# Kernel optimization log

Hardware: AMD Instinct MI355X
Metric: run time of the kernel (lower is better)

The kernel has to match this reference:

```python
import jax, jax.numpy as jnp
from jax import lax
import numpy as np

NEG = -1e9  # -inf surrogate for DP boundaries (matches deepblast's large-negative init)


def _lstm(xe, W_ih, W_hh, b):
    # xe: (B, T, D) -> hidden states (B, T, H). Single-layer LSTM via lax.scan.
    B, T, _ = xe.shape
    H = W_hh.shape[0]
    pre = xe @ W_ih + b  # precompute input contributions: (B, T, 4H)
    def step(carry, p):
        h, c = carry
        z = p + h @ W_hh
        i, f, g, o = jnp.split(z, 4, axis=-1)
        c = jax.nn.sigmoid(f) * c + jax.nn.sigmoid(i) * jnp.tanh(g)
        h = jax.nn.sigmoid(o) * jnp.tanh(c)
        return (h, c), h
    h0 = jnp.zeros((B, H), xe.dtype)
    _, hs = lax.scan(step, (h0, h0), jnp.swapaxes(pre, 0, 1))
    return jnp.swapaxes(hs, 0, 1)


def _embed(tok, emb, W_ih, W_hh, b_lstm, W_out, b_out):
    # StackedRNN: token embedding -> LSTM -> linear projection to nembed
    return _lstm(emb[tok], W_ih, W_hh, b_lstm) @ W_out + b_out


def _nw(theta, A):
    # Softmax-relaxed Needleman-Wunsch terminal value, anti-diagonal wavefront scan.
    # V[i,j] = theta[i-1,j-1] + logsumexp(V[i-1,j-1], V[i-1,j]+A, V[i,j-1]+A)
    B, N, M = theta.shape
    ii = jnp.arange(N + 1)
    d0 = jnp.full((B, N + 1), NEG, theta.dtype).at[:, 0].set(0.0)  # diag k=0: V[0,0]=0
    d1 = jnp.full((B, N + 1), NEG, theta.dtype)                    # diag k=1: boundaries
    def shift(a):  # a[i] -> a[i-1]
        return jnp.concatenate([jnp.full((a.shape[0], 1), NEG, a.dtype), a[:, :-1]], axis=1)
    def step(carry, k):
        p2, p1 = carry  # diagonals k-2, k-1; entry i holds V[i, (k-2)-i] / V[i, (k-1)-i]
        jj = k - ii
        valid = (ii >= 1) & (ii <= N) & (jj >= 1) & (jj <= M)
        td = theta[:, jnp.clip(ii - 1, 0, N - 1), jnp.clip(jj - 1, 0, M - 1)]  # (B, N+1)
        v = jax.nn.logsumexp(jnp.stack([shift(p1) + A, shift(p2), p1 + A], 0), axis=0)
        cur = jnp.where(valid[None, :], td + v, NEG)
        return (p1, cur), None
    (_, last), _ = lax.scan(step, (d0, d1), jnp.arange(2, N + M + 1))
    return last[:, N]  # V[N, M] per batch


def setup_inputs() -> dict:
    key = jax.random.key(0)
    ks = jax.random.split(key, 10)
    B, T, V, E, H = 32, 512, 22, 512, 512
    return {
        "x": jax.random.randint(ks[0], (B, T), 0, V),
        "y": jax.random.randint(ks[1], (B, T), 0, V),
        "emb": jax.random.normal(ks[2], (V, E), jnp.float32) * 0.1,
        "W_ih": jax.random.normal(ks[3], (E, 4 * H), jnp.float32) * 0.05,
        "W_hh": jax.random.normal(ks[4], (H, 4 * H), jnp.float32) * 0.05,
        "b_lstm": jnp.zeros((4 * H,), jnp.float32),
        "W_out": jax.random.normal(ks[5], (H, E), jnp.float32) * 0.05,
        "b_out": jnp.zeros((E,), jnp.float32),
        "W_gap": jax.random.normal(ks[6], (2 * E, 1), jnp.float32) * 0.05,
        "b_gap": jnp.zeros((1,), jnp.float32),
    }


def reference(x, y, emb, W_ih, W_hh, b_lstm, W_out, b_out, W_gap, b_gap):
    zx = _embed(x, emb, W_ih, W_hh, b_lstm, W_out, b_out)  # (B, N, E)
    zy = _embed(y, emb, W_ih, W_hh, b_lstm, W_out, b_out)  # (B, M, E)
    theta = jnp.einsum('bid,bjd->bij', zx, zy)             # (B, N, M)
    merged = jnp.concatenate([zx.mean(1), zy.mean(1)], axis=1)
    A = merged @ W_gap + b_gap                             # (B, 1) learned gap score
    return _nw(theta, A)                                   # (B,) DP terminal value
```

## Files before the change

kernel.cpp:

```cpp
#include <hip/hip_runtime.h>
#include <math.h>

#define TSEQ 512
#define HDIM 512
#define EDIM 512
#define NB   32
#define ROWS 64
#define GATES 2048
#define NEGV -1000000000.0f

typedef __attribute__((ext_vector_type(8))) short bf16x8;
typedef __attribute__((ext_vector_type(4))) float f32x4;

__device__ __forceinline__ float sigf(float x){ return __builtin_amdgcn_rcpf(1.0f + __expf(-x)); }

__device__ __forceinline__ float tanhfast(float x){
  float t = __expf(-2.0f*fabsf(x));
  float r = (1.0f - t)*__builtin_amdgcn_rcpf(1.0f + t);
  return copysignf(r, x);
}

__device__ __forceinline__ unsigned short f2bf(float f){
  unsigned int u = __builtin_bit_cast(unsigned int, f);
  unsigned int r = (u + 0x7fff + ((u>>16)&1)) >> 16;
  return (unsigned short)r;
}

__device__ __forceinline__ float bf2f(unsigned short v){
  unsigned int u = ((unsigned int)v)<<16;
  return __builtin_bit_cast(float, u);
}

__global__ __launch_bounds__(256) void table_k(const float* __restrict__ emb,
        const float* __restrict__ W_ih, const float* __restrict__ b_lstm,
        float* __restrict__ table){
  int j = blockIdx.x*256 + threadIdx.x;
  int v = blockIdx.y;
  float acc = b_lstm[j];
  #pragma unroll 4
  for(int k=0;k<EDIM;k++) acc = fmaf(emb[v*EDIM+k], W_ih[(size_t)k*GATES+j], acc);
  table[(size_t)v*GATES+j] = acc;
}

__global__ __launch_bounds__(64) void wprep_k(const float* __restrict__ W_hh,
        unsigned short* __restrict__ Wswz){
  int cid = blockIdx.x;
  int lane = threadIdx.x;
  int js = cid>>6, g = (cid>>4)&3, kc = cid&15;
  int col = g*512 + js*16 + (lane&15);
  int kbase = kc*32 + (lane>>4)*8;
  unsigned short v[8];
  #pragma unroll
  for(int e=0;e<8;e++) v[e] = f2bf(W_hh[(size_t)(kbase+e)*GATES + col]);
  *(uint4*)&Wswz[((size_t)cid*64 + lane)*8] = *(const uint4*)v;
}

__global__ __launch_bounds__(64) void wprep2_k(const float* __restrict__ W_out,
        unsigned short* __restrict__ wsw){
  int cid = blockIdx.x;
  int lane = threadIdx.x;
  int nc = cid>>4, kc = cid&15;
  int col = nc*16 + (lane&15);
  int kb = kc*32 + (lane>>4)*8;
  unsigned short v[8];
  #pragma unroll
  for(int e=0;e<8;e++) v[e] = f2bf(W_out[(size_t)(kb+e)*EDIM + col]);
  *(uint4*)&wsw[((size_t)cid*64 + lane)*8] = *(const uint4*)v;
}

__global__ __launch_bounds__(64,1) void lstm_wave(const int* __restrict__ x, const int* __restrict__ y,
        const float* __restrict__ table, const unsigned short* __restrict__ Wswz,
        unsigned* __restrict__ hx, unsigned short* __restrict__ hsb){
  __shared__ unsigned short wlds[8192];
  int w = blockIdx.x;
  int c = w>>6, mh = (w>>5)&1, js = w&31;
  int gid = c*2 + mh;
  int lane = threadIdx.x;

  bf16x8 wf[48];
  {
    const unsigned short* wp = Wswz + (size_t)js*32768;
    #pragma unroll
    for(int g=0;g<3;g++)
      #pragma unroll
      for(int kc=0;kc<16;kc++)
        wf[g*16+kc] = *(const bf16x8*)(const void*)&wp[((size_t)(g*16+kc)*64 + lane)*8];
  }
  {
    const uint4* src = (const uint4*)(Wswz + (size_t)js*32768 + 48*512);
    uint4* dst = (uint4*)wlds;
    #pragma unroll
    for(int i=0;i<16;i++) dst[lane + i*64] = src[lane + i*64];
  }
  __syncthreads();

  const int* tokbase = c ? y : x;
  int jloc = lane&15;
  int j    = js*16 + jloc;
  int hi   = (j>>3)&3;
  int kc_o = j>>5;
  int e_o  = j&7;
  int rl0  = (lane>>4)*4;
  unsigned pub_vo = (unsigned)(((kc_o*64 + (rl0|(hi<<4)))*8 + e_o)*4);
  int rbase = c*32 + mh*16 + rl0;
  float cst[4] = {0.f,0.f,0.f,0.f};

  unsigned* gbase = hx + (size_t)gid*16384;
  unsigned vo32 = (unsigned)lane*32u;
  int js_s = lane&31;
  unsigned sent_vo = (unsigned)((((js_s>>1)*512) + (js_s&1)*256)*4);

  for(int s=0;s<TSEQ;s++){
    const unsigned* hin = gbase + (size_t)(s&1)*8192;
    unsigned* hout      = gbase + (size_t)((s+1)&1)*8192;
    unsigned tagexp = (unsigned)s;

    float tb[4][4];
    {
      int toks[4];
      #pragma unroll
      for(int q=0;q<4;q++) toks[q] = tokbase[(mh*16 + rl0 + q)*TSEQ + s];
      #pragma unroll
      for(int q=0;q<4;q++){
        const float* tbl = table + (size_t)toks[q]*GATES;
        tb[0][q]=tbl[j]; tb[1][q]=tbl[512+j]; tb[2][q]=tbl[1024+j]; tb[3][q]=tbl[1536+j];
      }
    }

    while(true){
      unsigned sd;
      asm volatile(
        "global_load_dword %0, %1, %2 sc0 sc1\n\t"
        "s_waitcnt vmcnt(0)"
        : "=&v"(sd)
        : "v"(sent_vo), "s"((const void*)hin)
        : "memory");
      __builtin_amdgcn_sched_barrier(0);
      if(__all((int)((sd & 0xFFFFu) == tagexp))) break;
      __builtin_amdgcn_s_sleep(1);
    }

    uint4 ra[32];
    while(true){
      #pragma unroll
      for(int kc=0;kc<16;kc++){
        asm volatile(
          "global_load_dwordx4 %0, %2, %3 sc0 sc1\n\t"
          "global_load_dwordx4 %1, %2, %3 offset:16 sc0 sc1"
          : "=&v"(ra[2*kc]), "=&v"(ra[2*kc+1])
          : "v"(vo32), "s"((const void*)(hin + (size_t)kc*512))
          : "memory");
      }
      asm volatile("s_waitcnt vmcnt(0)" ::: "memory");
      __builtin_amdgcn_sched_barrier(0);
      unsigned acc = 0u;
      #pragma unroll
      for(int i=0;i<32;i++)
        acc |= (ra[i].x ^ tagexp) | (ra[i].y ^ tagexp) | (ra[i].z ^ tagexp) | (ra[i].w ^ tagexp);
      if(__all((int)((acc & 0xFFFFu) == 0u))) break;
      __builtin_amdgcn_s_sleep(1);
    }

    f32x4 acc0={0,0,0,0}, acc1={0,0,0,0}, acc2={0,0,0,0}, acc3={0,0,0,0};
    #pragma unroll
    for(int kc=0;kc<16;kc++){
      uint4 pk_;
      pk_.x = (ra[2*kc].x  >>16) | (ra[2*kc].y  & 0xFFFF0000u);
      pk_.y = (ra[2*kc].z  >>16) | (ra[2*kc].w  & 0xFFFF0000u);
      pk_.z = (ra[2*kc+1].x>>16) | (ra[2*kc+1].y& 0xFFFF0000u);
      pk_.w = (ra[2*kc+1].z>>16) | (ra[2*kc+1].w& 0xFFFF0000u);
      bf16x8 afk = __builtin_bit_cast(bf16x8, pk_);
      acc0 = __builtin_amdgcn_mfma_f32_16x16x32_bf16(afk, wf[kc],    acc0, 0,0,0);
      acc1 = __builtin_amdgcn_mfma_f32_16x16x32_bf16(afk, wf[16+kc], acc1, 0,0,0);
      acc2 = __builtin_amdgcn_mfma_f32_16x16x32_bf16(afk, wf[32+kc], acc2, 0,0,0);
      bf16x8 b3 = *(const bf16x8*)(const void*)&wlds[((size_t)kc*64 + lane)*8];
      acc3 = __builtin_amdgcn_mfma_f32_16x16x32_bf16(afk, b3,        acc3, 0,0,0);
    }

    unsigned hv[4]; unsigned short hb16[4];
    int sc = s>>4, sl = s&15;
    unsigned tagw = (unsigned)(s+1);
    #pragma unroll
    for(int q=0;q<4;q++){
      float zi = acc0[q] + tb[0][q];
      float zf = acc1[q] + tb[1][q];
      float zg = acc2[q] + tb[2][q];
      float zo = acc3[q] + tb[3][q];
      float cn = sigf(zf)*cst[q] + sigf(zi)*tanhfast(zg);
      float h  = sigf(zo)*tanhfast(cn);
      cst[q] = cn;
      unsigned short hbv = f2bf(h);
      hb16[q] = hbv;
      hv[q] = ((unsigned)hbv<<16) | tagw;
    }
    asm volatile(
      "global_store_dword %[a], %[d0], %[sb] sc0 sc1\n\t"
      "global_store_dword %[a], %[d1], %[sb] offset:32 sc0 sc1\n\t"
      "global_store_dword %[a], %[d2], %[sb] offset:64 sc0 sc1\n\t"
      "global_store_dword %[a], %[d3], %[sb] offset:96 sc0 sc1"
      :: [a]"v"(pub_vo), [d0]"v"(hv[0]),[d1]"v"(hv[1]),[d2]"v"(hv[2]),[d3]"v"(hv[3]),
         [sb]"s"((void*)hout)
      : "memory");
    #pragma unroll
    for(int q=0;q<4;q++){
      int r = rbase + q;
      int mc = r*32 + sc;
      hsb[((size_t)(mc*16 + kc_o)*64 + (sl|(hi<<4)))*8 + e_o] = hb16[q];
    }
  }
}

__global__ __launch_bounds__(256) void zproj_mfma(const unsigned short* __restrict__ hsb,
        const unsigned short* __restrict__ woutswz, const float* __restrict__ b_out,
        unsigned short* __restrict__ zxA, unsigned short* __restrict__ zyB,
        float* __restrict__ zmean){
  int tid = threadIdx.x, wv = tid>>6, lane = tid&63;
  int m0 = blockIdx.x*128 + (wv>>1)*64;
  int n0 = blockIdx.y*128 + (wv&1)*64;
  int mc0 = m0>>4, nc0 = n0>>4;
  const uint4* ha = (const uint4*)hsb;
  const uint4* wb = (const uint4*)woutswz;
  f32x4 acc[4][4];
  #pragma unroll
  for(int i=0;i<4;i++)
    #pragma unroll
    for(int k2=0;k2<4;k2++) acc[i][k2] = (f32x4){0,0,0,0};
  for(int kc=0;kc<16;kc++){
    bf16x8 a[4], b[4];
    #pragma unroll
    for(int i=0;i<4;i++){
      a[i] = __builtin_bit_cast(bf16x8, ha[((size_t)((mc0+i)*16 + kc))*64 + lane]);
      b[i] = __builtin_bit_cast(bf16x8, wb[((size_t)((nc0+i)*16 + kc))*64 + lane]);
    }
    #pragma unroll
    for(int mi=0;mi<4;mi++)
      #pragma unroll
      for(int ci=0;ci<4;ci++)
        acc[mi][ci] = __builtin_amdgcn_mfma_f32_16x16x32_bf16(a[mi], b[ci], acc[mi][ci], 0,0,0);
  }
  int r = m0>>9;
  bool isx = (r < NB);
  unsigned short* zb = isx ? zxA : zyB;
  int bb = isx ? r : r-NB;
  #pragma unroll
  for(int ci=0;ci<4;ci++){
    int n = n0 + ci*16 + (lane&15);
    float bo = b_out[n];
    int kcz = n>>5, hi = (n>>3)&3, ez = n&7;
    float colsum = 0.f;
    #pragma unroll
    for(int mi=0;mi<4;mi++){
      #pragma unroll
      for(int q=0;q<4;q++){
        int m = m0 + mi*16 + (lane>>4)*4 + q;
        float zv = acc[mi][ci][q] + bo;
        colsum += acc[mi][ci][q];
        int i = m&511;
        zb[(((size_t)(bb*32 + (i>>4))*16 + kcz)*64 + ((i&15)|(hi<<4)))*8 + ez] = f2bf(zv);
      }
    }
    colsum += __shfl_xor(colsum, 16);
    colsum += __shfl_xor(colsum, 32);
    if((lane>>4)==0) atomicAdd(&zmean[(size_t)r*EDIM + n], colsum);
  }
}

__global__ __launch_bounds__(256) void theta_mfma(const unsigned short* __restrict__ zxA,
        const unsigned short* __restrict__ zyB, unsigned short* __restrict__ th_n){
  int tid = threadIdx.x, wv = tid>>6, lane = tid&63;
  int b = blockIdx.z;
  int i0 = blockIdx.x*128 + (wv>>1)*64;
  int j0 = blockIdx.y*128 + (wv&1)*64;
  int ic0 = i0>>4, jc0 = j0>>4;
  const uint4* pa = (const uint4*)zxA;
  const uint4* pb = (const uint4*)zyB;
  f32x4 acc[4][4];
  #pragma unroll
  for(int i=0;i<4;i++)
    #pragma unroll
    for(int k2=0;k2<4;k2++) acc[i][k2] = (f32x4){0,0,0,0};
  for(int kc=0;kc<16;kc++){
    bf16x8 a[4], bfr[4];
    #pragma unroll
    for(int i=0;i<4;i++){
      a[i]   = __builtin_bit_cast(bf16x8, pa[((size_t)(b*32 + ic0+i)*16 + kc)*64 + lane]);
      bfr[i] = __builtin_bit_cast(bf16x8, pb[((size_t)(b*32 + jc0+i)*16 + kc)*64 + lane]);
    }
    #pragma unroll
    for(int mi=0;mi<4;mi++)
      #pragma unroll
      for(int ci=0;ci<4;ci++)
        acc[mi][ci] = __builtin_amdgcn_mfma_f32_16x16x32_bf16(a[mi], bfr[ci], acc[mi][ci], 0,0,0);
  }
  #pragma unroll
  for(int mi=0;mi<4;mi++){
    #pragma unroll
    for(int ci=0;ci<4;ci++){
      #pragma unroll
      for(int q=0;q<4;q++){
        int i  = i0 + mi*16 + (lane>>4)*4 + q;
        int jj = j0 + ci*16 + (lane&15);
        th_n[((size_t)b*TSEQ + i)*TSEQ + jj] = f2bf(acc[mi][ci][q]);
      }
    }
  }
}

#define DP 136
__global__ __launch_bounds__(128) void diag_k(const unsigned short* __restrict__ th_n,
        unsigned short* __restrict__ thD){
  __shared__ unsigned short t[128*DP];
  int b = blockIdx.z;
  int i0 = blockIdx.x*128;
  int j0 = blockIdx.y*128;
  int tid = threadIdx.x;
  {
    int cc = (tid&7)*16;
    for(int rr = tid>>3; rr<128; rr+=16){
      const uint4* src = (const uint4*)&th_n[((size_t)(b*TSEQ + i0+rr))*TSEQ + j0 + cc];
      uint4 v0 = src[0], v1 = src[1];
      *(uint4*)&t[rr*DP + cc]     = v0;
      *(uint4*)&t[rr*DP + cc + 8] = v1;
    }
  }
  __syncthreads();
  for(int u=0;u<255;u++){
    int d = i0 + j0 + u;
    int ibeg = (u>127) ? (d - j0 - 127) : i0;
    int iend = (u<128) ? (d - j0)       : (i0+127);
    int len = iend - ibeg + 1;
    if(tid < len){
      int i = ibeg + tid;
      thD[((size_t)b*1023 + d)*TSEQ + i] = t[(i-i0)*DP + (d-i-j0)];
    }
  }
}

__global__ __launch_bounds__(256) void gap_k(const float* __restrict__ zmean,
        const float* __restrict__ b_out, const float* __restrict__ W_gap,
        const float* __restrict__ b_gap, float* __restrict__ Aout){
  __shared__ float red[256];
  int b = blockIdx.x;
  int tid = threadIdx.x;
  float acc=0.f;
  for(int i=tid;i<2*EDIM;i+=256){
    int e = (i<EDIM)? i : i-EDIM;
    float msum = (i<EDIM)? zmean[(size_t)b*EDIM+e] : zmean[(size_t)(b+NB)*EDIM+e];
    float m = msum*(1.0f/TSEQ) + b_out[e];
    acc = fmaf(m, W_gap[i], acc);
  }
  red[tid]=acc; __syncthreads();
  for(int s=128;s>0;s>>=1){ if(tid<s) red[tid]+=red[tid+s]; __syncthreads(); }
  if(tid==0) Aout[b] = red[0] + b_gap[0];
}

__global__ __launch_bounds__(64) void nw_k(const unsigned short* __restrict__ thD,
        const float* __restrict__ Aout, float* __restrict__ out){
  const float L2E = 1.4426950408889634f, LN2 = 0.6931471805599453f;
  int b = blockIdx.x;
  int lane = threadIdx.x;
  float A = Aout[b];
  const unsigned short* thb = thD + (size_t)b*1023*TSEQ;
  float p1[8], p2[8];
  #pragma unroll
  for(int i=0;i<8;i++){ p1[i]=NEGV; p2[i]=NEGV; }
  float p1_0 = NEGV, p2_0 = 0.0f;
  uint4 t0 = *(const uint4*)&thb[(size_t)0*TSEQ + lane*8];
  uint4 t1 = *(const uint4*)&thb[(size_t)1*TSEQ + lane*8];
  uint4 t2 = *(const uint4*)&thb[(size_t)2*TSEQ + lane*8];
  uint4 t3 = *(const uint4*)&thb[(size_t)3*TSEQ + lane*8];
  uint4 t4 = *(const uint4*)&thb[(size_t)4*TSEQ + lane*8];
  uint4 t5 = *(const uint4*)&thb[(size_t)5*TSEQ + lane*8];
  uint4 t6 = *(const uint4*)&thb[(size_t)6*TSEQ + lane*8];
  uint4 t7 = *(const uint4*)&thb[(size_t)7*TSEQ + lane*8];
  int k = 2;

#define PF(row) ((size_t)((row)>1022?1022:(row))*TSEQ + lane*8)
#define NWCORE(TB) { \
    float td[8]; \
    td[0]=bf2f((unsigned short)(TB.x&0xFFFF)); td[1]=bf2f((unsigned short)(TB.x>>16)); \
    td[2]=bf2f((unsigned short)(TB.y&0xFFFF)); td[3]=bf2f((unsigned short)(TB.y>>16)); \
    td[4]=bf2f((unsigned short)(TB.z&0xFFFF)); td[5]=bf2f((unsigned short)(TB.z>>16)); \
    td[6]=bf2f((unsigned short)(TB.w&0xFFFF)); td[7]=bf2f((unsigned short)(TB.w>>16)); \
    float pm1 = __shfl_up(p1[7],1); \
    float pm2 = __shfl_up(p2[7],1); \
    if(lane==0){ pm1 = p1_0; pm2 = p2_0; } \
    float cur[8]; \
    _Pragma("unroll") \
    for(int cx=0;cx<8;cx++){ \
      int ii = lane*8+1+cx; \
      int jq = k-ii; \
      bool valid = (jq>=1)&&(jq<=512); \
      float a_ = (cx==0? pm1 : p1[cx-1]) + A; \
      float bb = (cx==0? pm2 : p2[cx-1]); \
      float cc = p1[cx] + A; \
      float mm = fmaxf(fmaxf(a_,bb),cc); \
      float sum = exp2f((a_-mm)*L2E) + exp2f((bb-mm)*L2E) + exp2f((cc-mm)*L2E); \
      float v = mm + log2f(sum)*LN2; \
      cur[cx] = valid ? td[cx] + v : NEGV; \
    } \
    _Pragma("unroll") \
    for(int cx=0;cx<8;cx++){ p2[cx]=p1[cx]; p1[cx]=cur[cx]; } \
    p2_0 = p1_0; p1_0 = NEGV; \
    k++; }

  for(int d0=0; d0<1016; d0+=8){
    NWCORE(t0); t0 = *(const uint4*)&thb[PF(d0+ 8)];
    NWCORE(t1); t1 = *(const uint4*)&thb[PF(d0+ 9)];
    NWCORE(t2); t2 = *(const uint4*)&thb[PF(d0+10)];
    NWCORE(t3); t3 = *(const uint4*)&thb[PF(d0+11)];
    NWCORE(t4); t4 = *(const uint4*)&thb[PF(d0+12)];
    NWCORE(t5); t5 = *(const uint4*)&thb[PF(d0+13)];
    NWCORE(t6); t6 = *(const uint4*)&thb[PF(d0+14)];
    NWCORE(t7); t7 = *(const uint4*)&thb[PF(d0+15)];
  }
  NWCORE(t0); NWCORE(t1); NWCORE(t2); NWCORE(t3);
  NWCORE(t4); NWCORE(t5); NWCORE(t6);
  if(lane==63) out[b] = p1[7];
#undef NWCORE
#undef PF
}

extern "C" void kernel_launch(void* const* d_in, const int* in_sizes, int n_in,
                              void* d_out, int out_size, void* d_ws, size_t ws_size,
                              hipStream_t stream) {
  (void)in_sizes; (void)n_in; (void)out_size; (void)ws_size;
  const int*   x      = (const int*)d_in[0];
  const int*   y      = (const int*)d_in[1];
  const float* emb    = (const float*)d_in[2];
  const float* W_ih   = (const float*)d_in[3];
  const float* W_hh   = (const float*)d_in[4];
  const float* b_lstm = (const float*)d_in[5];
  const float* W_out  = (const float*)d_in[6];
  const float* b_out  = (const float*)d_in[7];
  const float* W_gap  = (const float*)d_in[8];
  const float* b_gap  = (const float*)d_in[9];
  float* out = (float*)d_out;

  char* ws = (char*)d_ws;
  const size_t OFF_TABLE = 0;
  const size_t OFF_WSWZ  = 184320;
  const size_t OFF_WOUT  = OFF_WSWZ  + 2097152;
  const size_t OFF_HX    = OFF_WOUT  + 524288;
  const size_t OFF_HSB   = OFF_HX    + 262144;
  const size_t OFF_ZXA   = OFF_HSB   + 33554432;
  const size_t OFF_ZYB   = OFF_ZXA   + 16777216;
  const size_t OFF_THN   = OFF_ZYB   + 16777216;
  const size_t OFF_THD   = OFF_THN   + 33554432;
  const size_t OFF_ZMEAN = OFF_THD   + 33521664;
  const size_t OFF_AOUT  = OFF_ZMEAN + 131072;
  float* table = (float*)(ws + OFF_TABLE);
  unsigned short* Wswz    = (unsigned short*)(ws + OFF_WSWZ);
  unsigned short* woutswz = (unsigned short*)(ws + OFF_WOUT);
  unsigned* hx = (unsigned*)(ws + OFF_HX);
  unsigned short* hsb  = (unsigned short*)(ws + OFF_HSB);
  unsigned short* zxA  = (unsigned short*)(ws + OFF_ZXA);
  unsigned short* zyB  = (unsigned short*)(ws + OFF_ZYB);
  unsigned short* th_n = (unsigned short*)(ws + OFF_THN);
  unsigned short* thD  = (unsigned short*)(ws + OFF_THD);
  float* zmean = (float*)(ws + OFF_ZMEAN);
  float* Aout  = (float*)(ws + OFF_AOUT);

  hipMemsetAsync(hx, 0, 262144, stream);
  hipMemsetAsync(zmean, 0, 131072, stream);

  table_k<<<dim3(8,22), 256, 0, stream>>>(emb, W_ih, b_lstm, table);
  wprep_k<<<2048, 64, 0, stream>>>(W_hh, Wswz);
  wprep2_k<<<512, 64, 0, stream>>>(W_out, woutswz);
  lstm_wave<<<128, 64, 0, stream>>>(x, y, table, Wswz, hx, hsb);
  zproj_mfma<<<dim3(256,4), 256, 0, stream>>>(hsb, woutswz, b_out, zxA, zyB, zmean);
  theta_mfma<<<dim3(4,4,32), 256, 0, stream>>>(zxA, zyB, th_n);
  diag_k<<<dim3(4,4,32), 128, 0, stream>>>(th_n, thD);
  gap_k<<<32, 256, 0, stream>>>(zmean, b_out, W_gap, b_gap, Aout);
  nw_k<<<32, 64, 0, stream>>>(thD, Aout, out);
}
```

Measured before the change: 2.493 ms.

## Fuse theta GEMM with diagonal reorder and merge LSTM sentinel poll with data load

The theta MFMA kernel now writes its 128x128 tile into shared memory and emits the anti-diagonal layout directly, removing the separate diag_k launch and the 32MB th_n round trip through global memory. Separately, the LSTM step's sentinel poll and the hidden-state loads are issued together in one loop, so a step no longer pays a serial sentinel round trip before loading data. The trade-off is that while waiting, each poll iteration re-loads the full hidden vector, adding memory traffic, and the fused kernel has to fit the shared tile alongside its MFMA registers.

```diff
diff --git a/kernel.cpp b/kernel.cpp
--- a/kernel.cpp
+++ b/kernel.cpp
@@ -127,21 +127,14 @@
       }
     }
 
+    uint4 ra[32];
+    unsigned sd;
     while(true){
-      unsigned sd;
       asm volatile(
-        "global_load_dword %0, %1, %2 sc0 sc1\n\t"
-        "s_waitcnt vmcnt(0)"
+        "global_load_dword %0, %1, %2 sc0 sc1"
         : "=&v"(sd)
         : "v"(sent_vo), "s"((const void*)hin)
         : "memory");
-      __builtin_amdgcn_sched_barrier(0);
-      if(__all((int)((sd & 0xFFFFu) == tagexp))) break;
-      __builtin_amdgcn_s_sleep(1);
-    }
-
-    uint4 ra[32];
-    while(true){
       #pragma unroll
       for(int kc=0;kc<16;kc++){
         asm volatile(
@@ -153,11 +146,13 @@
       }
       asm volatile("s_waitcnt vmcnt(0)" ::: "memory");
       __builtin_amdgcn_sched_barrier(0);
-      unsigned acc = 0u;
-      #pragma unroll
-      for(int i=0;i<32;i++)
-        acc |= (ra[i].x ^ tagexp) | (ra[i].y ^ tagexp) | (ra[i].z ^ tagexp) | (ra[i].w ^ tagexp);
-      if(__all((int)((acc & 0xFFFFu) == 0u))) break;
+      if(__all((int)((sd & 0xFFFFu) == tagexp))){
+        unsigned acc = 0u;
+        #pragma unroll
+        for(int i=0;i<32;i++)
+          acc |= (ra[i].x ^ tagexp) | (ra[i].y ^ tagexp) | (ra[i].z ^ tagexp) | (ra[i].w ^ tagexp);
+        if(__all((int)((acc & 0xFFFFu) == 0u))) break;
+      }
       __builtin_amdgcn_s_sleep(1);
     }
 
@@ -265,13 +260,17 @@
   }
 }
 
-__global__ __launch_bounds__(256) void theta_mfma(const unsigned short* __restrict__ zxA,
-        const unsigned short* __restrict__ zyB, unsigned short* __restrict__ th_n){
+#define DP 136
+__global__ __launch_bounds__(256) void theta_diag_k(const unsigned short* __restrict__ zxA,
+        const unsigned short* __restrict__ zyB, unsigned short* __restrict__ thD){
+  __shared__ unsigned short t[128*DP];
   int tid = threadIdx.x, wv = tid>>6, lane = tid&63;
   int b = blockIdx.z;
-  int i0 = blockIdx.x*128 + (wv>>1)*64;
-  int j0 = blockIdx.y*128 + (wv&1)*64;
-  int ic0 = i0>>4, jc0 = j0>>4;
+  int i0 = blockIdx.x*128;
+  int j0 = blockIdx.y*128;
+  int iw = (wv>>1)*64;
+  int jw = (wv&1)*64;
+  int ic0 = (i0+iw)>>4, jc0 = (j0+jw)>>4;
   const uint4* pa = (const uint4*)zxA;
   const uint4* pb = (const uint4*)zyB;
   f32x4 acc[4][4];
@@ -298,40 +297,25 @@
     for(int ci=0;ci<4;ci++){
       #pragma unroll
       for(int q=0;q<4;q++){
-        int i  = i0 + mi*16 + (lane>>4)*4 + q;
-        int jj = j0 + ci*16 + (lane&15);
-        th_n[((size_t)b*TSEQ + i)*TSEQ + jj] = f2bf(acc[mi][ci][q]);
-      }
-    }
-  }
-}
-
-#define DP 136
-__global__ __launch_bounds__(128) void diag_k(const unsigned short* __restrict__ th_n,
-        unsigned short* __restrict__ thD){
-  __shared__ unsigned short t[128*DP];
-  int b = blockIdx.z;
-  int i0 = blockIdx.x*128;
-  int j0 = blockIdx.y*128;
-  int tid = threadIdx.x;
-  {
-    int cc = (tid&7)*16;
-    for(int rr = tid>>3; rr<128; rr+=16){
-      const uint4* src = (const uint4*)&th_n[((size_t)(b*TSEQ + i0+rr))*TSEQ + j0 + cc];
-      uint4 v0 = src[0], v1 = src[1];
-      *(uint4*)&t[rr*DP + cc]     = v0;
-      *(uint4*)&t[rr*DP + cc + 8] = v1;
+        int row = iw + mi*16 + (lane>>4)*4 + q;
+        int col = jw + ci*16 + (lane&15);
+        t[row*DP + col] = f2bf(acc[mi][ci][q]);
+      }
     }
   }
   __syncthreads();
-  for(int u=0;u<255;u++){
-    int d = i0 + j0 + u;
-    int ibeg = (u>127) ? (d - j0 - 127) : i0;
-    int iend = (u<128) ? (d - j0)       : (i0+127);
-    int len = iend - ibeg + 1;
-    if(tid < len){
-      int i = ibeg + tid;
-      thD[((size_t)b*1023 + d)*TSEQ + i] = t[(i-i0)*DP + (d-i-j0)];
+  int t2 = tid&127;
+  for(int u2=0;u2<256;u2+=2){
+    int u = u2 + (tid>>7);
+    if(u<255){
+      int d = i0 + j0 + u;
+      int ibeg = (u>127) ? (d - j0 - 127) : i0;
+      int iend = (u<128) ? (d - j0)       : (i0+127);
+      int len = iend - ibeg + 1;
+      if(t2 < len){
+        int i = ibeg + t2;
+        thD[((size_t)b*1023 + d)*TSEQ + i] = t[(i-i0)*DP + (d-i-j0)];
+      }
     }
   }
 }
@@ -445,8 +429,7 @@
   const size_t OFF_HSB   = OFF_HX    + 262144;
   const size_t OFF_ZXA   = OFF_HSB   + 33554432;
   const size_t OFF_ZYB   = OFF_ZXA   + 16777216;
-  const size_t OFF_THN   = OFF_ZYB   + 16777216;
-  const size_t OFF_THD   = OFF_THN   + 33554432;
+  const size_t OFF_THD   = OFF_ZYB   + 16777216;
   const size_t OFF_ZMEAN = OFF_THD   + 33521664;
   const size_t OFF_AOUT  = OFF_ZMEAN + 131072;
   float* table = (float*)(ws + OFF_TABLE);
@@ -456,7 +439,6 @@
   unsigned short* hsb  = (unsigned short*)(ws + OFF_HSB);
   unsigned short* zxA  = (unsigned short*)(ws + OFF_ZXA);
   unsigned short* zyB  = (unsigned short*)(ws + OFF_ZYB);
-  unsigned short* th_n = (unsigned short*)(ws + OFF_THN);
   unsigned short* thD  = (unsigned short*)(ws + OFF_THD);
   float* zmean = (float*)(ws + OFF_ZMEAN);
   float* Aout  = (float*)(ws + OFF_AOUT);
@@ -469,8 +451,7 @@
   wprep2_k<<<512, 64, 0, stream>>>(W_out, woutswz);
   lstm_wave<<<128, 64, 0, stream>>>(x, y, table, Wswz, hx, hsb);
   zproj_mfma<<<dim3(256,4), 256, 0, stream>>>(hsb, woutswz, b_out, zxA, zyB, zmean);
-  theta_mfma<<<dim3(4,4,32), 256, 0, stream>>>(zxA, zyB, th_n);
-  diag_k<<<dim3(4,4,32), 128, 0, stream>>>(th_n, thD);
+  theta_diag_k<<<dim3(4,4,32), 256, 0, stream>>>(zxA, zyB, thD);
   gap_k<<<32, 256, 0, stream>>>(zmean, b_out, W_gap, b_gap, Aout);
   nw_k<<<32, 64, 0, stream>>>(thD, Aout, out);
 }
```

Measured after the change: 2.758 ms. 10.6% more time.
